# Performance work log

Hardware: AMD Instinct MI355X
Metric: run time of the kernel (lower is better)

## Reference

```python
import jax, jax.numpy as jnp
import numpy as np

DIM = 512
HEADS = 8
HD = 64
FFN = 2048
WIN = 64            # cantor_local_window; also medium-scale stride
N_LOCAL = 64        # budget 128 * 0.5
N_MED = 38          # budget 128 * 0.3
N_GLOB = 26         # remainder (ratio 0.2)
EPS = 1e-5


def _indices(S):
    # Multi-scale O(n) sampling pattern: per-query key indices [S, K].
    pos = jnp.arange(S)[:, None]
    local = jnp.clip(pos + jnp.arange(N_LOCAL) - N_LOCAL // 2, 0, S - 1)
    med_off = (jnp.arange(N_MED) - N_MED // 2) * WIN
    medium = jnp.clip(pos + med_off, 0, S - 1)
    glob = jnp.linspace(0, S - 1, N_GLOB).astype(jnp.int32)
    glob = jnp.broadcast_to(glob[None, :], (S, N_GLOB))
    return jnp.concatenate([local, medium, glob], axis=1)


def _layernorm(x, g, b):
    mu = jnp.mean(x, axis=-1, keepdims=True)
    var = jnp.mean((x - mu) ** 2, axis=-1, keepdims=True)
    return (x - mu) * jax.lax.rsqrt(var + EPS) * g + b


def _cantor_attention(x, mask, wqkv, bqkv, wo, bo):
    B, S, D = x.shape
    qkv = x @ wqkv + bqkv                      # [B,S,3D]
    q, k, v = jnp.split(qkv, 3, axis=-1)
    heads = lambda t: t.reshape(B, S, HEADS, HD).transpose(0, 2, 1, 3)
    q, k, v = heads(q), heads(k), heads(v)     # [B,H,S,hd]
    idx = _indices(S)                          # [S,K]
    k_g = k[:, :, idx, :]                      # [B,H,S,K,hd]
    v_g = v[:, :, idx, :]
    scores = jnp.einsum('bhsd,bhskd->bhsk', q, k_g) / np.sqrt(HD).astype(np.float32)
    m_g = mask[:, idx]                         # [B,S,K]
    scores = jnp.where(m_g[:, None, :, :], scores, jnp.finfo(scores.dtype).min)
    attn = jax.nn.softmax(scores, axis=-1)
    out = jnp.einsum('bhsk,bhskd->bhsd', attn, v_g)
    out = out.transpose(0, 2, 1, 3).reshape(B, S, D)
    return out @ wo + bo


def setup_inputs() -> dict:
    key = jax.random.key(0)
    ks = jax.random.split(key, 8)
    s = lambda fan: 1.0 / np.sqrt(fan)
    return {
        'x': jax.random.normal(ks[0], (1, 2048, DIM), jnp.float32),
        'attention_mask': jnp.ones((1, 2048), jnp.bool_),
        'ln1_g': jnp.ones((DIM,), jnp.float32),
        'ln1_b': jnp.zeros((DIM,), jnp.float32),
        'ln2_g': jnp.ones((DIM,), jnp.float32),
        'ln2_b': jnp.zeros((DIM,), jnp.float32),
        'wqkv': jax.random.normal(ks[1], (DIM, 3 * DIM), jnp.float32) * s(DIM),
        'bqkv': jnp.zeros((3 * DIM,), jnp.float32),
        'wo': jax.random.normal(ks[2], (DIM, DIM), jnp.float32) * s(DIM),
        'bo': jnp.zeros((DIM,), jnp.float32),
        'w1': jax.random.normal(ks[3], (DIM, FFN), jnp.float32) * s(DIM),
        'b1': jnp.zeros((FFN,), jnp.float32),
        'w2': jax.random.normal(ks[4], (FFN, DIM), jnp.float32) * s(FFN),
        'b2': jnp.zeros((DIM,), jnp.float32),
    }


def reference(x, attention_mask, ln1_g, ln1_b, ln2_g, ln2_b,
              wqkv, bqkv, wo, bo, w1, b1, w2, b2):
    # pre-norm transformer block with Cantor O(n) attention (eval mode, dropout=0)
    attn_out = _cantor_attention(_layernorm(x, ln1_g, ln1_b), attention_mask,
                                 wqkv, bqkv, wo, bo)
    x = x + attn_out
    h = _layernorm(x, ln2_g, ln2_b)
    h = jax.nn.gelu(h @ w1 + b1, approximate=False) @ w2 + b2
    return x + h
```

## Files before the change

### kernel.cpp

```cpp
#include <hip/hip_runtime.h>
#include <math.h>

typedef float f32x4 __attribute__((ext_vector_type(4)));
typedef short s16x8 __attribute__((ext_vector_type(8)));
typedef unsigned short u16x8 __attribute__((ext_vector_type(8)));
typedef unsigned short ushort_t;
typedef unsigned int uint_t;

#define D_MODEL 512
#define N_HEADS 8
#define HEAD_D  64
#define D_FFN   2048

__device__ __forceinline__ float bf2f(unsigned short u) {
  union { unsigned int i; float f; } c; c.i = ((unsigned int)u) << 16; return c.f;
}
__device__ __forceinline__ unsigned short f2bf(float f) {
  union { float f; unsigned int i; } c; c.f = f;
  unsigned int x = c.i;
  return (unsigned short)((x + 0x7FFFu + ((x >> 16) & 1u)) >> 16);
}
__device__ __forceinline__ float ldx(const void* p, size_t i, int f) {
  return f ? ((const float*)p)[i] : bf2f(((const ushort_t*)p)[i]);
}

struct DetectArgs { const void* p[14]; int n[14]; };

__global__ __launch_bounds__(256)
void detect_all(DetectArgs a, int* __restrict__ flags) {
  __shared__ int cnt[2];
  const int b = blockIdx.x;
  const int t = threadIdx.x;
  if (b == 1) { if (t == 0) flags[1] = 0; return; }
  if (t == 0) { cnt[0] = 0; cnt[1] = 0; }
  __syncthreads();
  const int n_u32 = a.n[b] >> 1;
  const int sample = n_u32 < 256 ? n_u32 : 256;
  if (t < sample) {
    uint_t u = ((const uint_t*)a.p[b])[t];
    if (u != 0u) {
      atomicAdd(&cnt[0], 1);
      int e = (u >> 7) & 0xFF;
      if (e >= 0x70 && e <= 0x83) atomicAdd(&cnt[1], 1);
    }
  }
  __syncthreads();
  if (t == 0) flags[b] = (cnt[0] >= 32 && cnt[1] * 4 <= cnt[0]) ? 1 : 0;
}

struct WDesc { const void* src; ushort_t* dst; int Kd, Nd, flag, tile0; };

__global__ __launch_bounds__(256)
void wconv_kernel(WDesc w0, WDesc w1, WDesc w2, WDesc w3,
                  const int* __restrict__ flags) {
  __shared__ ushort_t tile[32][33];
  const int b = blockIdx.x;
  WDesc d = (b < w1.tile0) ? w0 : (b < w2.tile0) ? w1 : (b < w3.tile0) ? w2 : w3;
  const int lt = b - d.tile0;
  const int tn = d.Nd / 32;
  const int bk = lt / tn, bn = lt % tn;
  const int f = flags[d.flag];
  const int tx = threadIdx.x & 31, ty = threadIdx.x >> 5;
#pragma unroll
  for (int r = 0; r < 4; ++r) {
    int k = bk * 32 + ty * 4 + r;
    tile[ty * 4 + r][tx] = f2bf(ldx(d.src, (size_t)k * d.Nd + bn * 32 + tx, f));
  }
  __syncthreads();
#pragma unroll
  for (int r = 0; r < 4; ++r) {
    int n = bn * 32 + ty * 4 + r;
    d.dst[(size_t)n * d.Kd + bk * 32 + tx] = tile[tx][ty * 4 + r];
  }
}

__global__ __launch_bounds__(256)
void ln1_kernel(const void* __restrict__ x, const void* __restrict__ g,
                const void* __restrict__ b, ushort_t* __restrict__ out,
                const int* __restrict__ flags) {
  const int fx = flags[0], fg = flags[2], fb = flags[3];
  const int row = blockIdx.x * 4 + (threadIdx.x >> 6);
  const int lane = threadIdx.x & 63;
  float v[8], sum = 0.f, sq = 0.f;
#pragma unroll
  for (int i = 0; i < 8; ++i) {
    v[i] = ldx(x, (size_t)row * D_MODEL + lane * 8 + i, fx);
    sum += v[i]; sq += v[i] * v[i];
  }
#pragma unroll
  for (int o = 32; o > 0; o >>= 1) { sum += __shfl_xor(sum, o); sq += __shfl_xor(sq, o); }
  const float mu = sum * (1.0f / D_MODEL);
  const float var = sq * (1.0f / D_MODEL) - mu * mu;
  const float rstd = rsqrtf(var + 1e-5f);
#pragma unroll
  for (int i = 0; i < 8; ++i) {
    int c = lane * 8 + i;
    out[(size_t)row * D_MODEL + c] =
        f2bf((v[i] - mu) * rstd * ldx(g, c, fg) + ldx(b, c, fb));
  }
}

__global__ __launch_bounds__(256)
void ln2_kernel(const float* __restrict__ y, const void* __restrict__ g,
                const void* __restrict__ b, ushort_t* __restrict__ out,
                const int* __restrict__ flags) {
  const int fg = flags[4], fb = flags[5];
  const int row = blockIdx.x * 4 + (threadIdx.x >> 6);
  const int lane = threadIdx.x & 63;
  float v[8], sum = 0.f, sq = 0.f;
#pragma unroll
  for (int i = 0; i < 8; ++i) {
    v[i] = y[(size_t)row * D_MODEL + lane * 8 + i];
    sum += v[i]; sq += v[i] * v[i];
  }
#pragma unroll
  for (int o = 32; o > 0; o >>= 1) { sum += __shfl_xor(sum, o); sq += __shfl_xor(sq, o); }
  const float mu = sum * (1.0f / D_MODEL);
  const float var = sq * (1.0f / D_MODEL) - mu * mu;
  const float rstd = rsqrtf(var + 1e-5f);
#pragma unroll
  for (int i = 0; i < 8; ++i) {
    int c = lane * 8 + i;
    out[(size_t)row * D_MODEL + c] =
        f2bf((v[i] - mu) * rstd * ldx(g, c, fg) + ldx(b, c, fb));
  }
}

template <int BM, int BN, int EPI>
__global__ __launch_bounds__(256)
void gemm_bt(const ushort_t* __restrict__ A, int lda,
             const ushort_t* __restrict__ BT, int ldb, int K,
             const void* __restrict__ bias, int bias_off,
             const void* __restrict__ res,
             float* __restrict__ yacc,
             ushort_t* __restrict__ out_bf, int ldo,
             const int* __restrict__ flags, int ibias, int ires, int addb) {
  constexpr int BK = 64;
  constexpr int FM = BM / 32, FN = BN / 32;
  constexpr int AG = BM / 32, BG = BN / 32;
  __shared__ __attribute__((aligned(16))) ushort_t As[BM][72];
  __shared__ __attribute__((aligned(16))) ushort_t Bs[BN][72];

  const int t = threadIdx.x;
  const int lane = t & 63, wave = t >> 6;
  const int wm = wave >> 1, wn = wave & 1;
  const int q = lane >> 4, lm = lane & 15;
  const int m0 = blockIdx.y * BM, n0 = blockIdx.x * BN;
  const int srow = t >> 3, sslot = t & 7;

  f32x4 acc[FM][FN];
#pragma unroll
  for (int i = 0; i < FM; ++i)
#pragma unroll
    for (int j = 0; j < FN; ++j) acc[i][j] = (f32x4)(0.0f);

  u16x8 av[AG], bv[BG];

  auto gload = [&](int k0) {
#pragma unroll
    for (int r = 0; r < AG; ++r)
      av[r] = *(const u16x8*)(A + (size_t)(m0 + r * 32 + srow) * lda + k0 + sslot * 8);
#pragma unroll
    for (int r = 0; r < BG; ++r)
      bv[r] = *(const u16x8*)(BT + (size_t)(n0 + r * 32 + srow) * ldb + k0 + sslot * 8);
  };
  auto swrite = [&]() {
#pragma unroll
    for (int r = 0; r < AG; ++r) *(u16x8*)&As[r * 32 + srow][sslot * 8] = av[r];
#pragma unroll
    for (int r = 0; r < BG; ++r) *(u16x8*)&Bs[r * 32 + srow][sslot * 8] = bv[r];
  };
  auto frag_mfma = [&](int kh) {
    s16x8 af[FM], bf[FN];
#pragma unroll
    for (int i = 0; i < FM; ++i)
      af[i] = *(const s16x8*)&As[wm * (BM / 2) + i * 16 + lm][kh * 32 + q * 8];
#pragma unroll
    for (int j = 0; j < FN; ++j)
      bf[j] = *(const s16x8*)&Bs[wn * (BN / 2) + j * 16 + lm][kh * 32 + q * 8];
#pragma unroll
    for (int i = 0; i < FM; ++i)
#pragma unroll
      for (int j = 0; j < FN; ++j)
        acc[i][j] = __builtin_amdgcn_mfma_f32_16x16x32_bf16(af[i], bf[j], acc[i][j], 0, 0, 0);
  };

  gload(0);
  swrite();
  __syncthreads();
  for (int k0 = BK; k0 < K; k0 += BK) {
    gload(k0);
    frag_mfma(0);
    frag_mfma(1);
    __syncthreads();
    swrite();
    __syncthreads();
  }
  frag_mfma(0);
  frag_mfma(1);

  const int fbias = flags[ibias];
#pragma unroll
  for (int i = 0; i < FM; ++i) {
#pragma unroll
    for (int j = 0; j < FN; ++j) {
      const int colg = n0 + wn * (BN / 2) + j * 16 + lm;
      float bb = 0.0f;
      if (EPI <= 2 || addb) bb = ldx(bias, bias_off + colg, fbias);
#pragma unroll
      for (int r = 0; r < 4; ++r) {
        const int rowg = m0 + wm * (BM / 2) + i * 16 + q * 4 + r;
        float v = acc[i][j][r] + bb;
        const size_t off = (size_t)rowg * ldo + colg;
        if constexpr (EPI == 0) {
          out_bf[off] = f2bf(v);
        } else if constexpr (EPI == 1) {
          out_bf[off] = f2bf(0.5f * v * (1.0f + erff(v * 0.70710678f)));
        } else if constexpr (EPI == 2) {
          yacc[off] = v + ldx(res, off, flags[ires]);
        } else if constexpr (EPI == 3) {
          yacc[off] += v;
        } else {
          float fin = yacc[off] + v;
          if (flags[ires]) ((float*)(void*)out_bf)[off] = fin;
          else             out_bf[off] = f2bf(fin);
        }
      }
    }
  }
}

template <int BM, int BN, int EPI>
__global__ __launch_bounds__(256)
void gemm_nn(const ushort_t* __restrict__ A, int lda, int K,
             const void* __restrict__ B, int ldb, int brow0, int bcol0,
             const void* __restrict__ bias, int bias_off,
             const void* __restrict__ res,
             float* __restrict__ yacc,
             ushort_t* __restrict__ out_bf, int ldo,
             const int* __restrict__ flags, int iB, int ibias, int ires, int addb) {
  constexpr int BK = 32;
  constexpr int FM = BM / 32, FN = BN / 32;
  __shared__ __attribute__((aligned(16))) ushort_t As[BM][40];
  __shared__ ushort_t Bs[BK][BN + 2];
  const int t = threadIdx.x;
  const int lane = t & 63, wave = t >> 6;
  const int wm = wave >> 1, wn = wave & 1;
  const int m0 = blockIdx.y * BM, n0 = blockIdx.x * BN;
  const int fB = flags[iB], fbias = flags[ibias];
  f32x4 acc[FM][FN];
#pragma unroll
  for (int i = 0; i < FM; ++i)
#pragma unroll
    for (int j = 0; j < FN; ++j) acc[i][j] = (f32x4)(0.0f);
  const int q = lane >> 4, lm = lane & 15;
  const int arow_s = t >> 2, aslot = t & 3;
  for (int k0 = 0; k0 < K; k0 += BK) {
    __syncthreads();
#pragma unroll
    for (int r = 0; r < BM / 64; ++r) {
      int row = r * 64 + arow_s;
      *(u16x8*)&As[row][aslot * 8] =
          *(const u16x8*)(A + (size_t)(m0 + row) * lda + k0 + aslot * 8);
    }
#pragma unroll
    for (int e = 0; e < (BK * BN) / 256; ++e) {
      int id = e * 256 + t;
      int k = id / BN, n = id % BN;
      Bs[k][n] = f2bf(ldx(B, (size_t)(brow0 + k0 + k) * ldb + bcol0 + n0 + n, fB));
    }
    __syncthreads();
    s16x8 af[FM], bf[FN];
#pragma unroll
    for (int i = 0; i < FM; ++i)
      af[i] = *(const s16x8*)&As[wm * (BM / 2) + i * 16 + lm][q * 8];
#pragma unroll
    for (int j = 0; j < FN; ++j) {
      int nl = wn * (BN / 2) + j * 16 + lm;
      u16x8 tmp;
#pragma unroll
      for (int f = 0; f < 8; ++f) tmp[f] = Bs[q * 8 + f][nl];
      bf[j] = __builtin_bit_cast(s16x8, tmp);
    }
#pragma unroll
    for (int i = 0; i < FM; ++i)
#pragma unroll
      for (int j = 0; j < FN; ++j)
        acc[i][j] = __builtin_amdgcn_mfma_f32_16x16x32_bf16(af[i], bf[j], acc[i][j], 0, 0, 0);
  }
#pragma unroll
  for (int i = 0; i < FM; ++i) {
#pragma unroll
    for (int j = 0; j < FN; ++j) {
      const int col = wn * (BN / 2) + j * 16 + lm;
      float bb = 0.0f;
      if (EPI != 3 || addb) bb = ldx(bias, bias_off + n0 + col, fbias);
#pragma unroll
      for (int r = 0; r < 4; ++r) {
        const int rowg = m0 + wm * (BM / 2) + i * 16 + q * 4 + r;
        float v = acc[i][j][r] + bb;
        if constexpr (EPI == 0) {
          out_bf[(size_t)rowg * ldo + n0 + col] = f2bf(v);
        } else if constexpr (EPI == 1) {
          out_bf[(size_t)rowg * ldo + n0 + col] =
              f2bf(0.5f * v * (1.0f + erff(v * 0.70710678f)));
        } else if constexpr (EPI == 2) {
          const size_t off = (size_t)rowg * D_MODEL + n0 + col;
          yacc[off] = v + ldx(res, off, flags[ires]);
        } else {
          const size_t off = (size_t)rowg * D_MODEL + n0 + col;
          yacc[off] += v;
        }
      }
    }
  }
}

__device__ __forceinline__ int key_index(int s, int j, int S) {
  int p;
  if (j < 64)       p = s + j - 32;
  else if (j < 102) p = s + (j - 83) * 64;
  else {
    int g = j - 102;
    p = (g == 25) ? (S - 1) : (int)(((double)g * (double)(S - 1)) / 25.0);
  }
  return min(max(p, 0), S - 1);
}

__global__ __launch_bounds__(256, 4)
void attn_kernel(const ushort_t* __restrict__ qkv, ushort_t* __restrict__ out, int S) {
  __shared__ float qs[4][64];
  __shared__ float ps[4][128];
  __shared__ int   offs[4][128];
  const int wave = threadIdx.x >> 6, lane = threadIdx.x & 63;
  const int pair = blockIdx.x * 4 + wave;
  const int h = pair / S;
  const int s = pair - h * S;

  const int i1 = key_index(s, lane, S);
  const int i2 = key_index(s, lane + 64, S);
  offs[wave][lane] = i1 * (3 * D_MODEL);
  offs[wave][lane + 64] = i2 * (3 * D_MODEL);
  qs[wave][lane] = bf2f(qkv[(size_t)s * (3 * D_MODEL) + h * HEAD_D + lane]);
  __syncthreads();

  const ushort_t* kb = qkv + D_MODEL + h * HEAD_D;
  const ushort_t* k1 = kb + (size_t)i1 * (3 * D_MODEL);
  const ushort_t* k2 = kb + (size_t)i2 * (3 * D_MODEL);
  u16x8 ka[8], kc[8];
#pragma unroll
  for (int c = 0; c < 8; ++c) {
    ka[c] = *(const u16x8*)(k1 + c * 8);
    kc[c] = *(const u16x8*)(k2 + c * 8);
  }
  float d1 = 0.f, d2 = 0.f;
#pragma unroll
  for (int c = 0; c < 8; ++c) {
#pragma unroll
    for (int e = 0; e < 8; ++e) {
      float qv = qs[wave][c * 8 + e];
      d1 += qv * bf2f(ka[c][e]);
      d2 += qv * bf2f(kc[c][e]);
    }
  }
  d1 *= 0.125f; d2 *= 0.125f;
  float mx = fmaxf(d1, d2);
#pragma unroll
  for (int o = 32; o > 0; o >>= 1) mx = fmaxf(mx, __shfl_xor(mx, o));
  const float e1 = __expf(d1 - mx), e2 = __expf(d2 - mx);
  float sm = e1 + e2;
#pragma unroll
  for (int o = 32; o > 0; o >>= 1) sm += __shfl_xor(sm, o);
  const float inv = 1.0f / sm;
  ps[wave][lane] = e1 * inv;
  ps[wave][lane + 64] = e2 * inv;
  __syncthreads();

  const int g = lane >> 3, d8 = (lane & 7) * 8;
  const ushort_t* vbase = qkv + 2 * D_MODEL + h * HEAD_D + d8;
  float oacc[8];
#pragma unroll
  for (int e = 0; e < 8; ++e) oacc[e] = 0.f;

  u16x8 vv[8];
  float pp[8];
#pragma unroll
  for (int st = 0; st < 8; ++st) {
    int j = st * 8 + g;
    vv[st] = *(const u16x8*)(vbase + offs[wave][j]);
    pp[st] = ps[wave][j];
  }
#pragma unroll
  for (int jb = 0; jb < 16; ++jb) {
    u16x8 cv = vv[jb & 7];
    float cp = pp[jb & 7];
    if (jb < 8) {
      int j = (jb + 8) * 8 + g;
      vv[jb & 7] = *(const u16x8*)(vbase + offs[wave][j]);
      pp[jb & 7] = ps[wave][j];
    }
#pragma unroll
    for (int e = 0; e < 8; ++e) oacc[e] += cp * bf2f(cv[e]);
  }
#pragma unroll
  for (int m = 8; m <= 32; m <<= 1)
#pragma unroll
    for (int e = 0; e < 8; ++e) oacc[e] += __shfl_xor(oacc[e], m);

  if (lane < 8) {
    u16x8 ov;
#pragma unroll
    for (int e = 0; e < 8; ++e) ov[e] = f2bf(oacc[e]);
    *(u16x8*)(out + (size_t)s * D_MODEL + h * HEAD_D + d8) = ov;
  }
}

__global__ __launch_bounds__(256)
void convert_kernel(const float* __restrict__ y, void* __restrict__ out,
                    const int* __restrict__ flags, int n) {
  const int fout = flags[0];
  int i = blockIdx.x * 256 + threadIdx.x;
  if (i < n) {
    float v = y[i];
    if (fout) ((float*)out)[i] = v;
    else      ((ushort_t*)out)[i] = f2bf(v);
  }
}

extern "C" void kernel_launch(void* const* d_in, const int* in_sizes, int n_in,
                              void* d_out, int out_size, void* d_ws, size_t ws_size,
                              hipStream_t stream) {
  const int S = in_sizes[0] / D_MODEL;
  const size_t sD = (size_t)S * D_MODEL;
  char* ws = (char*)d_ws;

  DetectArgs da;
  for (int i = 0; i < 14; ++i) { da.p[i] = d_in[i]; da.n[i] = in_sizes[i]; }

  ushort_t* h1    = (ushort_t*)d_out;
  ushort_t* attnb = (ushort_t*)d_out;
  ushort_t* h2    = (ushort_t*)d_out;

  const size_t MB = 1024 * 1024;
  if (ws_size >= 12 * MB + 64) {
    ushort_t* qkv   = (ushort_t*)ws;
    float*    y     = (float*)ws;
    ushort_t* gbuf  = (ushort_t*)(ws + 4 * MB);
    ushort_t* wqkvT = (ushort_t*)(ws + 6 * MB);
    ushort_t* woT   = (ushort_t*)(ws + 7 * MB + 512 * 1024);
    ushort_t* w1T   = (ushort_t*)(ws + 8 * MB);
    ushort_t* w2T   = (ushort_t*)(ws + 10 * MB);
    int*      flags = (int*)(ws + 12 * MB);

    detect_all<<<14, 256, 0, stream>>>(da, flags);

    WDesc dq  = { d_in[6],  wqkvT, D_MODEL, 3 * D_MODEL, 6,  0 };
    WDesc dwo = { d_in[8],  woT,   D_MODEL, D_MODEL,     8,  768 };
    WDesc dw1 = { d_in[10], w1T,   D_MODEL, D_FFN,       10, 1024 };
    WDesc dw2 = { d_in[12], w2T,   D_FFN,   D_MODEL,     12, 2048 };
    wconv_kernel<<<3072, 256, 0, stream>>>(dq, dwo, dw1, dw2, flags);

    ln1_kernel<<<S / 4, 256, 0, stream>>>(d_in[0], d_in[2], d_in[3], h1, flags);

    gemm_bt<64, 64, 0><<<dim3(24, S / 64), 256, 0, stream>>>(
        h1, D_MODEL, wqkvT, D_MODEL, D_MODEL, d_in[7], 0,
        nullptr, nullptr, qkv, 3 * D_MODEL, flags, 7, 0, 1);

    attn_kernel<<<(S * N_HEADS) / 4, 256, 0, stream>>>(qkv, attnb, S);

    gemm_bt<64, 64, 2><<<dim3(8, S / 64), 256, 0, stream>>>(
        attnb, D_MODEL, woT, D_MODEL, D_MODEL, d_in[9], 0,
        d_in[0], y, nullptr, D_MODEL, flags, 9, 0, 1);

    ln2_kernel<<<S / 4, 256, 0, stream>>>(y, d_in[4], d_in[5], h2, flags);

    const int Nc = D_FFN / 2;
    gemm_bt<64, 64, 1><<<dim3(Nc / 64, S / 64), 256, 0, stream>>>(
        h2, D_MODEL, w1T, D_MODEL, D_MODEL,
        d_in[11], 0, nullptr, nullptr, gbuf, Nc, flags, 11, 0, 1);
    gemm_bt<64, 64, 3><<<dim3(8, S / 64), 256, 0, stream>>>(
        gbuf, Nc, w2T, D_FFN, Nc, d_in[13], 0,
        nullptr, y, nullptr, D_MODEL, flags, 13, 0, 1);
    gemm_bt<64, 64, 1><<<dim3(Nc / 64, S / 64), 256, 0, stream>>>(
        h2, D_MODEL, w1T + (size_t)Nc * D_MODEL, D_MODEL, D_MODEL,
        d_in[11], Nc, nullptr, nullptr, gbuf, Nc, flags, 11, 0, 1);
    gemm_bt<64, 64, 4><<<dim3(8, S / 64), 256, 0, stream>>>(
        gbuf, Nc, w2T + (size_t)Nc, D_FFN, Nc, d_in[13], 0,
        nullptr, y, (ushort_t*)d_out, D_MODEL, flags, 13, 0, 0);
  } else {
    int P;
    if      (ws_size >= 12ull * MB + 4096) P = 1;
    else if (ws_size >=  8ull * MB + 4096) P = 2;
    else                                   P = 4;
    const int Nc = D_FFN / P;
    const size_t gbuf_bytes = (size_t)S * Nc * 2;
    const size_t qkv_bytes  = 3 * sD * 2;
    const size_t fo = 4ull * sD + gbuf_bytes;
    const size_t flags_pos = (qkv_bytes > fo ? qkv_bytes : fo);

    ushort_t* qkv  = (ushort_t*)ws;
    float*    y    = (float*)ws;
    ushort_t* gbuf = (ushort_t*)(ws + 4 * sD);
    int*      flags = (int*)(ws + flags_pos);

    detect_all<<<14, 256, 0, stream>>>(da, flags);
    ln1_kernel<<<S / 4, 256, 0, stream>>>(d_in[0], d_in[2], d_in[3], h1, flags);
    gemm_nn<128, 128, 0><<<dim3((3 * D_MODEL) / 128, S / 128), 256, 0, stream>>>(
        h1, D_MODEL, D_MODEL, d_in[6], 3 * D_MODEL, 0, 0, d_in[7], 0,
        nullptr, nullptr, qkv, 3 * D_MODEL, flags, 6, 7, 0, 1);
    attn_kernel<<<(S * N_HEADS) / 4, 256, 0, stream>>>(qkv, attnb, S);
    gemm_nn<64, 64, 2><<<dim3(D_MODEL / 64, S / 64), 256, 0, stream>>>(
        attnb, D_MODEL, D_MODEL, d_in[8], D_MODEL, 0, 0, d_in[9], 0,
        d_in[0], y, nullptr, D_MODEL, flags, 8, 9, 0, 1);
    ln2_kernel<<<S / 4, 256, 0, stream>>>(y, d_in[4], d_in[5], h2, flags);
    for (int p = 0; p < P; ++p) {
      if (Nc >= 1024) {
        gemm_nn<128, 128, 1><<<dim3(Nc / 128, S / 128), 256, 0, stream>>>(
            h2, D_MODEL, D_MODEL, d_in[10], D_FFN, 0, p * Nc, d_in[11], p * Nc,
            nullptr, nullptr, gbuf, Nc, flags, 10, 11, 0, 1);
      } else {
        gemm_nn<64, 64, 1><<<dim3(Nc / 64, S / 64), 256, 0, stream>>>(
            h2, D_MODEL, D_MODEL, d_in[10], D_FFN, 0, p * Nc, d_in[11], p * Nc,
            nullptr, nullptr, gbuf, Nc, flags, 10, 11, 0, 1);
      }
      gemm_nn<64, 64, 3><<<dim3(D_MODEL / 64, S / 64), 256, 0, stream>>>(
          gbuf, Nc, Nc, d_in[12], D_MODEL, p * Nc, 0, d_in[13], 0,
          nullptr, y, nullptr, D_MODEL, flags, 12, 13, 0, p == 0 ? 1 : 0);
    }
    convert_kernel<<<(int)((sD + 255) / 256), 256, 0, stream>>>(y, d_out, flags, (int)sD);
  }
}
```

Before: 221.8 us.

## Restructure attention QK stage to coalesced 8-lane-per-key layout without LDS

The score stage now assigns each key to a group of 8 lanes, each holding 8 head-dim elements, instead of one lane loading a whole 64-element key row. Partial dot products are reduced with three xor shuffles. Probabilities and key offsets stay in registers, which removes the shared-memory arrays and both block barriers. The aim is coalesced 16-byte K loads and less LDS and sync traffic. The cost is more shuffles and more registers per lane (16 offsets and 16 probabilities), which may hurt occupancy.

```diff
diff --git a/kernel.cpp b/kernel.cpp
--- a/kernel.cpp
+++ b/kernel.cpp
@@ -329,78 +329,70 @@
 
 __global__ __launch_bounds__(256, 4)
 void attn_kernel(const ushort_t* __restrict__ qkv, ushort_t* __restrict__ out, int S) {
-  __shared__ float qs[4][64];
-  __shared__ float ps[4][128];
-  __shared__ int   offs[4][128];
   const int wave = threadIdx.x >> 6, lane = threadIdx.x & 63;
   const int pair = blockIdx.x * 4 + wave;
   const int h = pair / S;
   const int s = pair - h * S;
-
-  const int i1 = key_index(s, lane, S);
-  const int i2 = key_index(s, lane + 64, S);
-  offs[wave][lane] = i1 * (3 * D_MODEL);
-  offs[wave][lane + 64] = i2 * (3 * D_MODEL);
-  qs[wave][lane] = bf2f(qkv[(size_t)s * (3 * D_MODEL) + h * HEAD_D + lane]);
-  __syncthreads();
-
-  const ushort_t* kb = qkv + D_MODEL + h * HEAD_D;
-  const ushort_t* k1 = kb + (size_t)i1 * (3 * D_MODEL);
-  const ushort_t* k2 = kb + (size_t)i2 * (3 * D_MODEL);
-  u16x8 ka[8], kc[8];
-#pragma unroll
-  for (int c = 0; c < 8; ++c) {
-    ka[c] = *(const u16x8*)(k1 + c * 8);
-    kc[c] = *(const u16x8*)(k2 + c * 8);
-  }
-  float d1 = 0.f, d2 = 0.f;
-#pragma unroll
-  for (int c = 0; c < 8; ++c) {
-#pragma unroll
-    for (int e = 0; e < 8; ++e) {
-      float qv = qs[wave][c * 8 + e];
-      d1 += qv * bf2f(ka[c][e]);
-      d2 += qv * bf2f(kc[c][e]);
-    }
-  }
-  d1 *= 0.125f; d2 *= 0.125f;
-  float mx = fmaxf(d1, d2);
-#pragma unroll
-  for (int o = 32; o > 0; o >>= 1) mx = fmaxf(mx, __shfl_xor(mx, o));
-  const float e1 = __expf(d1 - mx), e2 = __expf(d2 - mx);
-  float sm = e1 + e2;
-#pragma unroll
-  for (int o = 32; o > 0; o >>= 1) sm += __shfl_xor(sm, o);
+  const int g = lane >> 3, d8 = (lane & 7) * 8;
+
+  int koff[16];
+#pragma unroll
+  for (int r = 0; r < 16; ++r)
+    koff[r] = key_index(s, r * 8 + g, S) * (3 * D_MODEL);
+
+  u16x8 qv8 = *(const u16x8*)(qkv + (size_t)s * (3 * D_MODEL) + h * HEAD_D + d8);
+  float qf[8];
+#pragma unroll
+  for (int e = 0; e < 8; ++e) qf[e] = bf2f(qv8[e]);
+
+  const ushort_t* kbase = qkv + D_MODEL + h * HEAD_D + d8;
+  float pr[16];
+  {
+    u16x8 kv[8];
+#pragma unroll
+    for (int r = 0; r < 8; ++r) kv[r] = *(const u16x8*)(kbase + koff[r]);
+#pragma unroll
+    for (int r = 0; r < 16; ++r) {
+      u16x8 cur = kv[r & 7];
+      if (r < 8) kv[r & 7] = *(const u16x8*)(kbase + koff[r + 8]);
+      float d = 0.f;
+#pragma unroll
+      for (int e = 0; e < 8; ++e) d += qf[e] * bf2f(cur[e]);
+      d += __shfl_xor(d, 1);
+      d += __shfl_xor(d, 2);
+      d += __shfl_xor(d, 4);
+      pr[r] = d * 0.125f;
+    }
+  }
+
+  float mx = pr[0];
+#pragma unroll
+  for (int r = 1; r < 16; ++r) mx = fmaxf(mx, pr[r]);
+#pragma unroll
+  for (int m = 8; m <= 32; m <<= 1) mx = fmaxf(mx, __shfl_xor(mx, m));
+  float sm = 0.f;
+#pragma unroll
+  for (int r = 0; r < 16; ++r) { pr[r] = __expf(pr[r] - mx); sm += pr[r]; }
+#pragma unroll
+  for (int m = 8; m <= 32; m <<= 1) sm += __shfl_xor(sm, m);
   const float inv = 1.0f / sm;
-  ps[wave][lane] = e1 * inv;
-  ps[wave][lane + 64] = e2 * inv;
-  __syncthreads();
-
-  const int g = lane >> 3, d8 = (lane & 7) * 8;
+
   const ushort_t* vbase = qkv + 2 * D_MODEL + h * HEAD_D + d8;
   float oacc[8];
 #pragma unroll
   for (int e = 0; e < 8; ++e) oacc[e] = 0.f;
-
-  u16x8 vv[8];
-  float pp[8];
-#pragma unroll
-  for (int st = 0; st < 8; ++st) {
-    int j = st * 8 + g;
-    vv[st] = *(const u16x8*)(vbase + offs[wave][j]);
-    pp[st] = ps[wave][j];
-  }
-#pragma unroll
-  for (int jb = 0; jb < 16; ++jb) {
-    u16x8 cv = vv[jb & 7];
-    float cp = pp[jb & 7];
-    if (jb < 8) {
-      int j = (jb + 8) * 8 + g;
-      vv[jb & 7] = *(const u16x8*)(vbase + offs[wave][j]);
-      pp[jb & 7] = ps[wave][j];
-    }
-#pragma unroll
-    for (int e = 0; e < 8; ++e) oacc[e] += cp * bf2f(cv[e]);
+  {
+    u16x8 vv[8];
+#pragma unroll
+    for (int r = 0; r < 8; ++r) vv[r] = *(const u16x8*)(vbase + koff[r]);
+#pragma unroll
+    for (int r = 0; r < 16; ++r) {
+      u16x8 cv = vv[r & 7];
+      float cp = pr[r] * inv;
+      if (r < 8) vv[r & 7] = *(const u16x8*)(vbase + koff[r + 8]);
+#pragma unroll
+      for (int e = 0; e < 8; ++e) oacc[e] += cp * bf2f(cv[e]);
+    }
   }
 #pragma unroll
   for (int m = 8; m <= 32; m <<= 1)
```

Result: faster. 207.3 us (-6.6%).
